# Performance work log

Measured on AMD Instinct MI355X. Metric: run time of the kernel, lower is better.

Reference implementation:

```python
import jax, jax.numpy as jnp
import numpy as np

N_LEVELS = 8
N_FEATS = 2
LOG2_T = 19
BASE_RES = 16.0
FINEST_RES = 2048.0
BOX_MIN, BOX_MAX = 0.0, 1.0
B_GROWTH = float(np.exp((np.log(FINEST_RES) - np.log(BASE_RES)) / (N_LEVELS - 1)))  # = 2.0
HASH_MASK = (1 << LOG2_T) - 1
BATCH = 4194304


def setup_inputs() -> dict:
    key = jax.random.key(0)
    kx, kt = jax.random.split(key)
    x = jax.random.uniform(kx, (BATCH, 1), dtype=jnp.float32, minval=BOX_MIN, maxval=BOX_MAX)
    # n_levels separate embedding tables, init uniform in [-1e-4, 1e-4]
    tables = jax.random.uniform(kt, (N_LEVELS, 1 << LOG2_T, N_FEATS), dtype=jnp.float32,
                                minval=-1e-4, maxval=1e-4)
    return {"x": x, "tables": tables}


def reference(x, tables):
    # x: [B, 1] in [BOX_MIN, BOX_MAX]; tables: [L, 2^T, F]
    outs = []
    for i in range(N_LEVELS):
        resolution = jnp.floor(BASE_RES * (B_GROWTH ** i))
        grid_size = (BOX_MAX - BOX_MIN) / resolution
        idx = jnp.floor((x - BOX_MIN) / grid_size)            # [B, 1] cell index (float)
        interval_min = BOX_MIN + idx * grid_size              # [B, 1]
        interval_max = interval_min + grid_size               # [B, 1]
        # two interval vertices: idx and idx+1; 1-D spatial hash = index & (2^T - 1)
        verts = jnp.concatenate([idx, idx + 1.0], axis=-1).astype(jnp.int32)  # [B, 2]
        hashed = jnp.bitwise_and(verts, HASH_MASK)            # [B, 2]
        emb = tables[i][hashed]                               # [B, 2, F] gather
        w = (x - interval_min) / (interval_max - interval_min)  # [B, 1]
        c = emb[:, 0] * (1.0 - w) + emb[:, 1] * w             # [B, F]
        outs.append(c)
    return jnp.concatenate(outs, axis=-1)                     # [B, L*F]
```

## Files before the change

kernel.cpp:

```cpp
#include <hip/hip_runtime.h>


#define NGP_BATCH   4194304
#define NGP_TSIZE   (1 << 19)
#define BLOCK       512
#define PPB         8192
#define KITER       (PPB / (BLOCK/4))

typedef float f32x4 __attribute__((ext_vector_type(4)));

__global__ __launch_bounds__(BLOCK) void hashenc_kernel(
    const float* __restrict__ x,
    const float* __restrict__ tables,
    float* __restrict__ out)
{
    __shared__ float4 sm4[4080];

    const int tid = threadIdx.x;

#pragma unroll
    for (int l = 0; l < 8; ++l) {
        const int n   = 16 << l;
        const int off = 16 * ((1 << l) - 1);
        const float2* __restrict__ src =
            reinterpret_cast<const float2*>(tables) + (size_t)l * NGP_TSIZE;
        for (int e = tid; e < n; e += BLOCK) {
            const float2 a = src[e];
            const float2 b = src[e + 1];
            sm4[off + e] = make_float4(a.x, a.y, b.x, b.y);
        }
    }
    __syncthreads();

    const int q  = tid >> 2;
    const int s  = tid & 3;
    const int l0 = 2 * s;
    const int l1 = 2 * s + 1;
    const float res0 = (float)(16 << l0);
    const float res1 = (float)(16 << l1);
    const int   off0 = 16 * ((1 << l0) - 1);
    const int   off1 = 16 * ((1 << l1) - 1);

    const int P0 = blockIdx.x * PPB;
    f32x4* __restrict__ out4 = reinterpret_cast<f32x4*>(out);

#pragma unroll 4
    for (int k = 0; k < KITER; ++k) {
        const int   p  = P0 + q + 128 * k;
        const float xv = x[p];

        const float fx0 = xv * res0;
        const float fi0 = floorf(fx0);
        const float w0  = fx0 - fi0;
        const float4 e0 = sm4[off0 + (int)fi0];

        const float fx1 = xv * res1;
        const float fi1 = floorf(fx1);
        const float w1  = fx1 - fi1;
        const float4 e1 = sm4[off1 + (int)fi1];

        f32x4 r;
        r.x = e0.x * (1.0f - w0) + e0.z * w0;
        r.y = e0.y * (1.0f - w0) + e0.w * w0;
        r.z = e1.x * (1.0f - w1) + e1.z * w1;
        r.w = e1.y * (1.0f - w1) + e1.w * w1;

        __builtin_nontemporal_store(r, &out4[(size_t)p * 4 + s]);
    }
}

extern "C" void kernel_launch(void* const* d_in, const int* in_sizes, int n_in,
                              void* d_out, int out_size, void* d_ws, size_t ws_size,
                              hipStream_t stream) {
    const float* x      = (const float*)d_in[0];
    const float* tables = (const float*)d_in[1];
    float*       out    = (float*)d_out;

    const int grid = NGP_BATCH / PPB;
    hashenc_kernel<<<grid, BLOCK, 0, stream>>>(x, tables, out);
}
```

Before: 57.35 us.

## Halve shared-memory table footprint and raise occupancy with smaller per-block work

Shared memory now holds the tables as plain float2 entries (one per vertex, plus a trailing vertex) instead of pre-paired float4 cells. This halves LDS usage from about 64KB to 32KB per block so more blocks can be resident. Each lookup now does two float2 LDS reads instead of one float4. Points per block drop to 4096, the unroll factor drops to 2 and launch bounds request 8 waves per EU, which trades more table-preload overhead per block for higher occupancy to hide latency in this store-bound kernel.

```diff
diff --git a/kernel.cpp b/kernel.cpp
--- a/kernel.cpp
+++ b/kernel.cpp
@@ -4,31 +4,28 @@
 #define NGP_BATCH   4194304
 #define NGP_TSIZE   (1 << 19)
 #define BLOCK       512
-#define PPB         8192
+#define PPB         4096
 #define KITER       (PPB / (BLOCK/4))
 
 typedef float f32x4 __attribute__((ext_vector_type(4)));
 
-__global__ __launch_bounds__(BLOCK) void hashenc_kernel(
+__global__ __launch_bounds__(BLOCK, 8) void hashenc_kernel(
     const float* __restrict__ x,
     const float* __restrict__ tables,
     float* __restrict__ out)
 {
-    __shared__ float4 sm4[4080];
+    __shared__ float2 sm[4088];
 
     const int tid = threadIdx.x;
 
 #pragma unroll
     for (int l = 0; l < 8; ++l) {
-        const int n   = 16 << l;
-        const int off = 16 * ((1 << l) - 1);
+        const int n   = (16 << l) + 1;
+        const int off = 16 * ((1 << l) - 1) + l;
         const float2* __restrict__ src =
             reinterpret_cast<const float2*>(tables) + (size_t)l * NGP_TSIZE;
-        for (int e = tid; e < n; e += BLOCK) {
-            const float2 a = src[e];
-            const float2 b = src[e + 1];
-            sm4[off + e] = make_float4(a.x, a.y, b.x, b.y);
-        }
+        for (int e = tid; e < n; e += BLOCK)
+            sm[off + e] = src[e];
     }
     __syncthreads();
 
@@ -38,13 +35,13 @@
     const int l1 = 2 * s + 1;
     const float res0 = (float)(16 << l0);
     const float res1 = (float)(16 << l1);
-    const int   off0 = 16 * ((1 << l0) - 1);
-    const int   off1 = 16 * ((1 << l1) - 1);
+    const int   off0 = 16 * ((1 << l0) - 1) + l0;
+    const int   off1 = 16 * ((1 << l1) - 1) + l1;
 
     const int P0 = blockIdx.x * PPB;
     f32x4* __restrict__ out4 = reinterpret_cast<f32x4*>(out);
 
-#pragma unroll 4
+#pragma unroll 2
     for (int k = 0; k < KITER; ++k) {
         const int   p  = P0 + q + 128 * k;
         const float xv = x[p];
@@ -52,18 +49,22 @@
         const float fx0 = xv * res0;
         const float fi0 = floorf(fx0);
         const float w0  = fx0 - fi0;
-        const float4 e0 = sm4[off0 + (int)fi0];
+        const int   i0  = off0 + (int)fi0;
+        const float2 a0 = sm[i0];
+        const float2 b0 = sm[i0 + 1];
 
         const float fx1 = xv * res1;
         const float fi1 = floorf(fx1);
         const float w1  = fx1 - fi1;
-        const float4 e1 = sm4[off1 + (int)fi1];
+        const int   i1  = off1 + (int)fi1;
+        const float2 a1 = sm[i1];
+        const float2 b1 = sm[i1 + 1];
 
         f32x4 r;
-        r.x = e0.x * (1.0f - w0) + e0.z * w0;
-        r.y = e0.y * (1.0f - w0) + e0.w * w0;
-        r.z = e1.x * (1.0f - w1) + e1.z * w1;
-        r.w = e1.y * (1.0f - w1) + e1.w * w1;
+        r.x = a0.x * (1.0f - w0) + b0.x * w0;
+        r.y = a0.y * (1.0f - w0) + b0.y * w0;
+        r.z = a1.x * (1.0f - w1) + b1.x * w1;
+        r.w = a1.y * (1.0f - w1) + b1.y * w1;
 
         __builtin_nontemporal_store(r, &out4[(size_t)p * 4 + s]);
     }
```

Result: no change. 57.49 us (+0.2%).
